# Kernel optimization log

Hardware: AMD Instinct MI355X
Metric: run time of the kernel (lower is better)

## Reference

```python
import jax, jax.numpy as jnp
import numpy as np

HIDDEN = 2048
N_HEADS = 32
N_KV_HEADS = 8
HEAD_DIM = 64
ROPE_THETA = 500000.0
B, S = 1, 2048


def _rope_tables(seq_len):
    inv_freq = 1.0 / ROPE_THETA ** (jnp.arange(0, HEAD_DIM, 2, dtype=jnp.float32) / HEAD_DIM)
    angles = jnp.arange(seq_len, dtype=jnp.float32)[:, None] * inv_freq[None, :]
    return jnp.cos(angles), jnp.sin(angles)


def _apply_rope(x, cos, sin):
    # x: (B, S, H, D); cos/sin: (S, D//2)
    x1 = x[..., 0::2]
    x2 = x[..., 1::2]
    c = cos[None, :, None, :]
    s = sin[None, :, None, :]
    x1r = x1 * c - x2 * s
    x2r = x1 * s + x2 * c
    return jnp.stack([x1r, x2r], axis=-1).reshape(x.shape)


def setup_inputs() -> dict:
    key = jax.random.key(0)
    ks = jax.random.split(key, 5)
    hidden_states = jax.random.normal(ks[0], (B, S, HIDDEN), dtype=jnp.float32)
    # causal mask, broadcastable over (B, H, S, S)
    attention_mask = jnp.tril(jnp.ones((S, S), dtype=bool))[None, :, :]
    sc = 1.0 / np.sqrt(HIDDEN)
    wq = jax.random.normal(ks[1], (HIDDEN, N_HEADS * HEAD_DIM), dtype=jnp.float32) * sc
    wk = jax.random.normal(ks[2], (HIDDEN, N_KV_HEADS * HEAD_DIM), dtype=jnp.float32) * sc
    wv = jax.random.normal(ks[3], (HIDDEN, N_KV_HEADS * HEAD_DIM), dtype=jnp.float32) * sc
    wo = jax.random.normal(ks[4], (N_HEADS * HEAD_DIM, HIDDEN), dtype=jnp.float32) * sc
    return {"hidden_states": hidden_states, "attention_mask": attention_mask,
            "wq": wq, "wk": wk, "wv": wv, "wo": wo}


def reference(hidden_states, attention_mask, wq, wk, wv, wo):
    b, s, _ = hidden_states.shape
    groups = N_HEADS // N_KV_HEADS
    q = (hidden_states @ wq).reshape(b, s, N_HEADS, HEAD_DIM)
    k = (hidden_states @ wk).reshape(b, s, N_KV_HEADS, HEAD_DIM)
    v = (hidden_states @ wv).reshape(b, s, N_KV_HEADS, HEAD_DIM)
    cos, sin = _rope_tables(s)
    q = _apply_rope(q, cos, sin)
    k = _apply_rope(k, cos, sin)
    k = jnp.repeat(k, groups, axis=2)  # (b, s, H, D)
    v = jnp.repeat(v, groups, axis=2)
    q = q.transpose(0, 2, 1, 3)  # (b, H, s, D)
    k = k.transpose(0, 2, 1, 3)
    v = v.transpose(0, 2, 1, 3)
    scores = jnp.einsum('bhqd,bhkd->bhqk', q, k) / jnp.sqrt(jnp.float32(HEAD_DIM))
    scores = jnp.where(attention_mask[:, None, :, :], scores, -jnp.inf)
    probs = jax.nn.softmax(scores, axis=-1)
    out = jnp.einsum('bhqk,bhkd->bhqd', probs, v)
    out = out.transpose(0, 2, 1, 3).reshape(b, s, N_HEADS * HEAD_DIM)
    return out @ wo
```

## Files before the change

### kernel.cpp

```cpp
#include <hip/hip_runtime.h>

typedef __attribute__((ext_vector_type(8))) short short8;
typedef __attribute__((ext_vector_type(4))) float float4v;

__device__ __forceinline__ float bf2f(ushort u) {
    union { uint i; float f; } v; v.i = ((uint)u) << 16; return v.f;
}
__device__ __forceinline__ ushort f2bf(float f) {
    union { uint i; float f; } v; v.f = f;
    return (ushort)((v.i + 0x7FFFu + ((v.i >> 16) & 1u)) >> 16);
}
#if __has_builtin(__builtin_amdgcn_cvt_pk_bf16_f32)
__device__ __forceinline__ uint f2bf_pk(float a, float b) {
    auto r = __builtin_amdgcn_cvt_pk_bf16_f32(a, b);
    return __builtin_bit_cast(uint, r);
}
#else
__device__ __forceinline__ uint f2bf_pk(float a, float b) {
    return (uint)f2bf(a) | ((uint)f2bf(b) << 16);
}
#endif
__device__ __forceinline__ void gld_lds16(const ushort* g, ushort* l) {
    __builtin_amdgcn_global_load_lds((const __attribute__((address_space(1))) unsigned int*)g,
                                     (__attribute__((address_space(3))) unsigned int*)l,
                                     16, 0, 0);
}

__global__ __launch_bounds__(256) void cvt_bf16(const float* __restrict__ in,
                                                ushort* __restrict__ out) {
    const size_t i = ((size_t)blockIdx.x * 256 + threadIdx.x) * 8;
    float4 a = *(const float4*)(in + i);
    float4 b = *(const float4*)(in + i + 4);
    uint4 u;
    u.x = f2bf_pk(a.x, a.y);
    u.y = f2bf_pk(a.z, a.w);
    u.z = f2bf_pk(b.x, b.y);
    u.w = f2bf_pk(b.z, b.w);
    *(uint4*)(out + i) = u;
}

__device__ __forceinline__ void tconv_body(const float* in, ushort* out,
                                           int C, int r0, int c0, int tid) {
    __shared__ float t[64][65];
    const int lrow = tid >> 2;
    const int lc   = (tid & 3) * 16;

    const float* ip = in + (size_t)(r0 + lrow) * C + c0 + lc;
#pragma unroll
    for (int i = 0; i < 4; i++) {
        float4 v = *(const float4*)(ip + 4 * i);
        t[lrow][lc + 4 * i + 0] = v.x; t[lrow][lc + 4 * i + 1] = v.y;
        t[lrow][lc + 4 * i + 2] = v.z; t[lrow][lc + 4 * i + 3] = v.w;
    }
    __syncthreads();
    ushort* op = out + (size_t)(c0 + lrow) * 2048 + r0 + lc;
#pragma unroll
    for (int i = 0; i < 8; i++)
        ((uint*)op)[i] = f2bf_pk(t[lc + 2 * i][lrow], t[lc + 2 * i + 1][lrow]);
}

__global__ __launch_bounds__(256) void tconv(const float* __restrict__ in,
                                             ushort* __restrict__ out) {
    tconv_body(in, out, 2048, blockIdx.y * 64, blockIdx.x * 64, threadIdx.x);
}

__global__ __launch_bounds__(256) void tconv3(const float* __restrict__ wq,
                                              const float* __restrict__ wk,
                                              const float* __restrict__ wv,
                                              ushort* __restrict__ out) {
    const int bx = blockIdx.x;
    const float* in; ushort* op; int C, cx;
    if (bx < 32)      { in = wq; op = out;                          C = 2048; cx = bx; }
    else if (bx < 40) { in = wk; op = out + (size_t)2048 * 2048;    C = 512;  cx = bx - 32; }
    else              { in = wv; op = out + (size_t)2560 * 2048;    C = 512;  cx = bx - 40; }
    tconv_body(in, op, C, blockIdx.y * 64, cx * 64, threadIdx.x);
}

template <bool BF16OUT>
__global__ __launch_bounds__(256) void gemm_n64(const ushort* __restrict__ A,
                                                const ushort* __restrict__ Bt,
                                                void* __restrict__ Cout,
                                                int N, int K) {
    __shared__ ushort As[128 * 32];
    __shared__ ushort Bs[64 * 32];

    const int tid = threadIdx.x, w = tid >> 6, lane = tid & 63;
    const int lr = lane & 15, quad = lane >> 4;
    const int m0 = blockIdx.x * 128, n0 = blockIdx.y * 64;

    const int srow = lane >> 2;
    const int skb  = (lane & 3) ^ ((srow >> 1) & 3);

    float4v acc[2][4];
#pragma unroll
    for (int a = 0; a < 2; a++)
#pragma unroll
        for (int b = 0; b < 4; b++) { acc[a][b][0] = 0.f; acc[a][b][1] = 0.f; acc[a][b][2] = 0.f; acc[a][b][3] = 0.f; }

    const int fsw = (lr >> 1) & 3;

    for (int k0 = 0; k0 < K; k0 += 32) {
        __syncthreads();
#pragma unroll
        for (int i = 0; i < 2; i++) {
            const int rt = 2 * w + i;
            gld_lds16(A + (size_t)(m0 + rt * 16 + srow) * K + k0 + skb * 8, &As[rt * 512]);
        }
        gld_lds16(Bt + (size_t)(n0 + w * 16 + srow) * K + k0 + skb * 8, &Bs[w * 512]);
        __syncthreads();

        short8 af[2], bf[4];
#pragma unroll
        for (int mt = 0; mt < 2; mt++)
            af[mt] = *(const short8*)&As[(w * 32 + mt * 16 + lr) * 32 + (quad ^ fsw) * 8];
#pragma unroll
        for (int nt = 0; nt < 4; nt++)
            bf[nt] = *(const short8*)&Bs[(nt * 16 + lr) * 32 + (quad ^ fsw) * 8];
#pragma unroll
        for (int mt = 0; mt < 2; mt++)
#pragma unroll
            for (int nt = 0; nt < 4; nt++)
                acc[mt][nt] = __builtin_amdgcn_mfma_f32_16x16x32_bf16(af[mt], bf[nt], acc[mt][nt], 0, 0, 0);
    }

    const int rbase = m0 + w * 32 + quad * 4;
    const int cbase = n0 + lr;
#pragma unroll
    for (int mt = 0; mt < 2; mt++)
#pragma unroll
        for (int nt = 0; nt < 4; nt++)
#pragma unroll
            for (int r = 0; r < 4; r++) {
                const size_t idx = (size_t)(rbase + mt * 16 + r) * N + cbase + nt * 16;
                if (BF16OUT) ((ushort*)Cout)[idx] = f2bf(acc[mt][nt][r]);
                else         ((float*)Cout)[idx]  = acc[mt][nt][r];
            }
}

__global__ __launch_bounds__(256) void rope_bf(ushort* __restrict__ Qb,
                                               ushort* __restrict__ Kc) {
    const int idx = blockIdx.x * 256 + threadIdx.x;
    const int QP = 2048 * 1024;
    int s, p; ushort* base; float osc;
    if (idx < QP) { s = idx >> 10; p = idx & 1023; base = Qb; osc = 0.125f; }
    else { int r = idx - QP; s = r >> 8; p = r & 255; base = Kc; osc = 1.0f; }
    const int j = p & 31;
    float inv = __expf(-(float)(2 * j) * (1.0f / 64.0f) * 13.122363377404328f);
    float sn, c;
    sincosf((float)s * inv, &sn, &c);
    uint* p2 = (uint*)(base + (size_t)s * 3072 + 2 * p);
    uint xv = *p2;
    float x1 = bf2f((ushort)(xv & 0xFFFFu)), x2 = bf2f((ushort)(xv >> 16));
    *p2 = f2bf_pk((x1 * c - x2 * sn) * osc, (x1 * sn + x2 * c) * osc);
}

__global__ __launch_bounds__(256) void attn_mfma(const ushort* __restrict__ Q,
                                                 const ushort* __restrict__ Kc,
                                                 const ushort* __restrict__ Vc,
                                                 ushort* __restrict__ O) {
    __shared__ ushort Ks[2][64 * 64];
    __shared__ ushort Vt[2][64 * 72];
    __shared__ ushort Ps[4][16 * 72];

    const int tid = threadIdx.x, w = tid >> 6, lane = tid & 63;
    const int lr = lane & 15, quad = lane >> 4;
    const int h = blockIdx.y, g = h >> 2;

    const int dg = tid & 15;
    const int kl = tid >> 4;
    const int ksub = lane >> 3, dsub = lane & 7;
    ushort* Pw = &Ps[w][0];

    const ushort* Vp0 = Vc + g * 64 + dg * 4 + (size_t)3072 * kl;
    const ushort* Kp0 = Kc + g * 64 + ((dsub ^ ksub) * 8) + (size_t)3072 * ksub;

    short8 onesf;
#pragma unroll
    for (int j = 0; j < 8; j++) onesf[j] = (short)0x3F80;

    for (int ti = 0; ti < 2; ti++) {
        const int bx = ti ? 31 - (int)blockIdx.x : (int)blockIdx.x;

        const ushort* qp = Q + (size_t)(bx * 64 + w * 16 + lr) * 3072 + h * 64 + quad * 8;
        const short8 qf0 = *(const short8*)qp;
        const short8 qf1 = *(const short8*)(qp + 32);

        float4v oacc[4], lacc;
#pragma unroll
        for (int t = 0; t < 4; t++) { oacc[t][0] = 0.f; oacc[t][1] = 0.f; oacc[t][2] = 0.f; oacc[t][3] = 0.f; }
        lacc[0] = 0.f; lacc[1] = 0.f; lacc[2] = 0.f; lacc[3] = 0.f;

        uint2 vv[4];
#pragma unroll
        for (int t = 0; t < 4; t++)
            vv[t] = *(const uint2*)(Vp0 + (size_t)(16 * t) * 3072);
        __syncthreads();
#pragma unroll
        for (int i = 0; i < 2; i++) {
            const int rt = 2 * w + i;
            gld_lds16(Kp0 + (size_t)(rt * 8) * 3072, &Ks[0][rt * 512]);
        }

        for (int kb = 0; kb <= bx; kb++) {
            const int b = kb & 1;
            ushort* bKs = Ks[b];
            ushort* bVt = Vt[b];

#pragma unroll
            for (int i = 0; i < 4; i++) {
                uint e0 = (i < 2) ? vv[0].x : vv[0].y, f0 = (i & 1) ? (e0 >> 16) : (e0 & 0xFFFFu);
                uint e1 = (i < 2) ? vv[1].x : vv[1].y, f1 = (i & 1) ? (e1 >> 16) : (e1 & 0xFFFFu);
                uint e2 = (i < 2) ? vv[2].x : vv[2].y, f2 = (i & 1) ? (e2 >> 16) : (e2 & 0xFFFFu);
                uint e3 = (i < 2) ? vv[3].x : vv[3].y, f3 = (i & 1) ? (e3 >> 16) : (e3 & 0xFFFFu);
                uint2 pk; pk.x = f0 | (f1 << 16); pk.y = f2 | (f3 << 16);
                *(uint2*)&bVt[(dg * 4 + i) * 72 + kl * 4] = pk;
            }

            const int kn = (kb < bx) ? kb + 1 : bx;
#pragma unroll
            for (int t = 0; t < 4; t++)
                vv[t] = *(const uint2*)(Vp0 + (size_t)(kn * 64 + 16 * t) * 3072);

            asm volatile("s_waitcnt vmcnt(4) lgkmcnt(0)\n\ts_barrier" ::: "memory");

#pragma unroll
            for (int i = 0; i < 2; i++) {
                const int rt = 2 * w + i;
                gld_lds16(Kp0 + (size_t)(kn * 64 + rt * 8) * 3072, &Ks[1 - b][rt * 512]);
            }

            float4v sacc[4];
#pragma unroll
            for (int t = 0; t < 4; t++) { sacc[t][0] = 0.f; sacc[t][1] = 0.f; sacc[t][2] = 0.f; sacc[t][3] = 0.f; }
#pragma unroll
            for (int t = 0; t < 4; t++) {
                const int krow = t * 16 + lr;
                const int sw = lr & 7;
                short8 kf0 = *(const short8*)&bKs[krow * 64 + ((quad)     ^ sw) * 8];
                short8 kf1 = *(const short8*)&bKs[krow * 64 + ((quad + 4) ^ sw) * 8];
                sacc[t] = __builtin_amdgcn_mfma_f32_16x16x32_bf16(qf0, kf0, sacc[t], 0, 0, 0);
                sacc[t] = __builtin_amdgcn_mfma_f32_16x16x32_bf16(qf1, kf1, sacc[t], 0, 0, 0);
            }

            const bool mc = (kb == bx);
#pragma unroll
            for (int r = 0; r < 4; r++) {
                const int qr = w * 16 + quad * 4 + r;
                float p[4];
#pragma unroll
                for (int t = 0; t < 4; t++) {
                    float pv = __expf(sacc[t][r]);
                    p[t] = (mc && (t * 16 + lr > qr)) ? 0.f : pv;
                }
                uint2 pk;
                pk.x = f2bf_pk(p[0], p[1]);
                pk.y = f2bf_pk(p[2], p[3]);
                *(uint2*)&Pw[(quad * 4 + r) * 72 + lr * 4] = pk;
            }

#pragma unroll
            for (int ks2 = 0; ks2 < 2; ks2++) {
                short8 pf = *(const short8*)&Pw[lr * 72 + ks2 * 32 + quad * 8];
                lacc = __builtin_amdgcn_mfma_f32_16x16x32_bf16(pf, onesf, lacc, 0, 0, 0);
#pragma unroll
                for (int t = 0; t < 4; t++) {
                    short8 vf = *(const short8*)&bVt[(t * 16 + lr) * 72 + ks2 * 32 + quad * 8];
                    oacc[t] = __builtin_amdgcn_mfma_f32_16x16x32_bf16(pf, vf, oacc[t], 0, 0, 0);
                }
            }
        }

        ushort* op = O + (size_t)(bx * 64 + w * 16 + quad * 4) * 2048 + h * 64 + lr;
#pragma unroll
        for (int t = 0; t < 4; t++)
#pragma unroll
            for (int r = 0; r < 4; r++)
                op[(size_t)r * 2048 + t * 16] = f2bf(oacc[t][r] / lacc[r]);
    }
}

extern "C" void kernel_launch(void* const* d_in, const int* in_sizes, int n_in,
                              void* d_out, int out_size, void* d_ws, size_t ws_size,
                              hipStream_t stream) {
    const float* hidden = (const float*)d_in[0];
    const float* wq = (const float*)d_in[2];
    const float* wk = (const float*)d_in[3];
    const float* wv = (const float*)d_in[4];
    const float* wo = (const float*)d_in[5];

    ushort* ws = (ushort*)d_ws;
    ushort* hid  = ws;
    ushort* wT   = ws + 4194304;
    ushort* QKV  = ws + 10485760;
    ushort* Qb = QKV;
    ushort* Kc = QKV + 2048;
    ushort* Vc = QKV + 2560;
    ushort* Ab = hid;

    cvt_bf16<<<2048, 256, 0, stream>>>(hidden, hid);
    tconv3<<<dim3(48, 32), 256, 0, stream>>>(wq, wk, wv, wT);
    gemm_n64<true><<<dim3(16, 48), 256, 0, stream>>>(hid, wT, QKV, 3072, 2048);
    tconv<<<dim3(32, 32), 256, 0, stream>>>(wo, wT);
    rope_bf<<<10240, 256, 0, stream>>>(Qb, Kc);
    attn_mfma<<<dim3(16, 32), 256, 0, stream>>>(Qb, Kc, Vc, Ab);
    gemm_n64<false><<<dim3(16, 32), 256, 0, stream>>>(Ab, wT, d_out, 2048, 2048);
}
```

Before: 256.6 us.

## Split attention KV blocks across two partitions, merge prep kernels, swizzle LDS

```diff
diff --git a/kernel.cpp b/kernel.cpp
--- a/kernel.cpp
+++ b/kernel.cpp
@@ -2,6 +2,8 @@
 
 typedef __attribute__((ext_vector_type(8))) short short8;
 typedef __attribute__((ext_vector_type(4))) float float4v;
+
+union U4S8 { uint4 u; short8 s; };
 
 __device__ __forceinline__ float bf2f(ushort u) {
     union { uint i; float f; } v; v.i = ((uint)u) << 16; return v.f;
@@ -26,25 +28,11 @@
                                      16, 0, 0);
 }
 
-__global__ __launch_bounds__(256) void cvt_bf16(const float* __restrict__ in,
-                                                ushort* __restrict__ out) {
-    const size_t i = ((size_t)blockIdx.x * 256 + threadIdx.x) * 8;
-    float4 a = *(const float4*)(in + i);
-    float4 b = *(const float4*)(in + i + 4);
-    uint4 u;
-    u.x = f2bf_pk(a.x, a.y);
-    u.y = f2bf_pk(a.z, a.w);
-    u.z = f2bf_pk(b.x, b.y);
-    u.w = f2bf_pk(b.z, b.w);
-    *(uint4*)(out + i) = u;
-}
-
 __device__ __forceinline__ void tconv_body(const float* in, ushort* out,
                                            int C, int r0, int c0, int tid) {
     __shared__ float t[64][65];
     const int lrow = tid >> 2;
     const int lc   = (tid & 3) * 16;
-
     const float* ip = in + (size_t)(r0 + lrow) * C + c0 + lc;
 #pragma unroll
     for (int i = 0; i < 4; i++) {
@@ -59,28 +47,42 @@
         ((uint*)op)[i] = f2bf_pk(t[lc + 2 * i][lrow], t[lc + 2 * i + 1][lrow]);
 }
 
+__global__ __launch_bounds__(256) void prep(const float* __restrict__ hidden,
+                                            const float* __restrict__ wq,
+                                            const float* __restrict__ wk,
+                                            const float* __restrict__ wv,
+                                            ushort* __restrict__ hid,
+                                            ushort* __restrict__ wT) {
+    const int bx = blockIdx.x;
+    if (bx < 2048) {
+        const size_t i = ((size_t)bx * 256 + threadIdx.x) * 8;
+        float4 a = *(const float4*)(hidden + i);
+        float4 b = *(const float4*)(hidden + i + 4);
+        uint4 u;
+        u.x = f2bf_pk(a.x, a.y); u.y = f2bf_pk(a.z, a.w);
+        u.z = f2bf_pk(b.x, b.y); u.w = f2bf_pk(b.z, b.w);
+        *(uint4*)(hid + i) = u;
+    } else {
+        const int i = bx - 2048;
+        const int xx = i % 48, yy = i / 48;
+        const float* in; ushort* op; int C, cx;
+        if (xx < 32)      { in = wq; op = wT;                        C = 2048; cx = xx; }
+        else if (xx < 40) { in = wk; op = wT + (size_t)2048 * 2048;  C = 512;  cx = xx - 32; }
+        else              { in = wv; op = wT + (size_t)2560 * 2048;  C = 512;  cx = xx - 40; }
+        tconv_body(in, op, C, yy * 64, cx * 64, threadIdx.x);
+    }
+}
+
 __global__ __launch_bounds__(256) void tconv(const float* __restrict__ in,
                                              ushort* __restrict__ out) {
     tconv_body(in, out, 2048, blockIdx.y * 64, blockIdx.x * 64, threadIdx.x);
-}
-
-__global__ __launch_bounds__(256) void tconv3(const float* __restrict__ wq,
-                                              const float* __restrict__ wk,
-                                              const float* __restrict__ wv,
-                                              ushort* __restrict__ out) {
-    const int bx = blockIdx.x;
-    const float* in; ushort* op; int C, cx;
-    if (bx < 32)      { in = wq; op = out;                          C = 2048; cx = bx; }
-    else if (bx < 40) { in = wk; op = out + (size_t)2048 * 2048;    C = 512;  cx = bx - 32; }
-    else              { in = wv; op = out + (size_t)2560 * 2048;    C = 512;  cx = bx - 40; }
-    tconv_body(in, op, C, blockIdx.y * 64, cx * 64, threadIdx.x);
 }
 
 template <bool BF16OUT>
 __global__ __launch_bounds__(256) void gemm_n64(const ushort* __restrict__ A,
                                                 const ushort* __restrict__ Bt,
                                                 void* __restrict__ Cout,
-                                                int N, int K) {
+                                                int N, int K, int lda) {
     __shared__ ushort As[128 * 32];
     __shared__ ushort Bs[64 * 32];
 
@@ -104,7 +106,7 @@
 #pragma unroll
         for (int i = 0; i < 2; i++) {
             const int rt = 2 * w + i;
-            gld_lds16(A + (size_t)(m0 + rt * 16 + srow) * K + k0 + skb * 8, &As[rt * 512]);
+            gld_lds16(A + (size_t)(m0 + rt * 16 + srow) * lda + k0 + skb * 8, &As[rt * 512]);
         }
         gld_lds16(Bt + (size_t)(n0 + w * 16 + srow) * K + k0 + skb * 8, &Bs[w * 512]);
         __syncthreads();
@@ -142,7 +144,7 @@
     const int idx = blockIdx.x * 256 + threadIdx.x;
     const int QP = 2048 * 1024;
     int s, p; ushort* base; float osc;
-    if (idx < QP) { s = idx >> 10; p = idx & 1023; base = Qb; osc = 0.125f; }
+    if (idx < QP) { s = idx >> 10; p = idx & 1023; base = Qb; osc = 0.18033688f; }
     else { int r = idx - QP; s = r >> 8; p = r & 255; base = Kc; osc = 1.0f; }
     const int j = p & 31;
     float inv = __expf(-(float)(2 * j) * (1.0f / 64.0f) * 13.122363377404328f);
@@ -157,19 +159,24 @@
 __global__ __launch_bounds__(256) void attn_mfma(const ushort* __restrict__ Q,
                                                  const ushort* __restrict__ Kc,
                                                  const ushort* __restrict__ Vc,
-                                                 ushort* __restrict__ O) {
+                                                 ushort* __restrict__ O0,
+                                                 ushort* __restrict__ O1,
+                                                 float* __restrict__ L0,
+                                                 float* __restrict__ L1) {
     __shared__ ushort Ks[2][64 * 64];
-    __shared__ ushort Vt[2][64 * 72];
-    __shared__ ushort Ps[4][16 * 72];
+    __shared__ ushort Vt[2][64 * 64];
+    __shared__ ushort Ps[4][16 * 64];
 
     const int tid = threadIdx.x, w = tid >> 6, lane = tid & 63;
     const int lr = lane & 15, quad = lane >> 4;
-    const int h = blockIdx.y, g = h >> 2;
+    const int h = blockIdx.y, g = h >> 2, z = blockIdx.z;
 
     const int dg = tid & 15;
     const int kl = tid >> 4;
     const int ksub = lane >> 3, dsub = lane & 7;
-    ushort* Pw = &Ps[w][0];
+    ushort* Pw = Ps[w];
+    ushort* Op = z ? O1 : O0;
+    float*  Lp = z ? L1 : L0;
 
     const ushort* Vp0 = Vc + g * 64 + dg * 4 + (size_t)3072 * kl;
     const ushort* Kp0 = Kc + g * 64 + ((dsub ^ ksub) * 8) + (size_t)3072 * ksub;
@@ -180,6 +187,8 @@
 
     for (int ti = 0; ti < 2; ti++) {
         const int bx = ti ? 31 - (int)blockIdx.x : (int)blockIdx.x;
+        const int nch = (bx >= z) ? ((bx - z) >> 1) + 1 : 0;
+        const int last = z + 2 * (nch - 1);
 
         const ushort* qp = Q + (size_t)(bx * 64 + w * 16 + lr) * 3072 + h * 64 + quad * 8;
         const short8 qf0 = *(const short8*)qp;
@@ -191,32 +200,40 @@
         lacc[0] = 0.f; lacc[1] = 0.f; lacc[2] = 0.f; lacc[3] = 0.f;
 
         uint2 vv[4];
-#pragma unroll
-        for (int t = 0; t < 4; t++)
-            vv[t] = *(const uint2*)(Vp0 + (size_t)(16 * t) * 3072);
+        if (nch) {
+#pragma unroll
+            for (int t = 0; t < 4; t++)
+                vv[t] = *(const uint2*)(Vp0 + (size_t)(z * 64 + 16 * t) * 3072);
+        }
         __syncthreads();
-#pragma unroll
-        for (int i = 0; i < 2; i++) {
-            const int rt = 2 * w + i;
-            gld_lds16(Kp0 + (size_t)(rt * 8) * 3072, &Ks[0][rt * 512]);
-        }
-
-        for (int kb = 0; kb <= bx; kb++) {
-            const int b = kb & 1;
+        if (nch) {
+#pragma unroll
+            for (int i = 0; i < 2; i++) {
+                const int rt = 2 * w + i;
+                gld_lds16(Kp0 + (size_t)(z * 64 + rt * 8) * 3072, &Ks[0][rt * 512]);
+            }
+        }
+
+        for (int c = 0; c < nch; c++) {
+            const int kb = z + 2 * c;
+            const int b = c & 1;
             ushort* bKs = Ks[b];
             ushort* bVt = Vt[b];
 
 #pragma unroll
             for (int i = 0; i < 4; i++) {
-                uint e0 = (i < 2) ? vv[0].x : vv[0].y, f0 = (i & 1) ? (e0 >> 16) : (e0 & 0xFFFFu);
-                uint e1 = (i < 2) ? vv[1].x : vv[1].y, f1 = (i & 1) ? (e1 >> 16) : (e1 & 0xFFFFu);
-                uint e2 = (i < 2) ? vv[2].x : vv[2].y, f2 = (i & 1) ? (e2 >> 16) : (e2 & 0xFFFFu);
-                uint e3 = (i < 2) ? vv[3].x : vv[3].y, f3 = (i & 1) ? (e3 >> 16) : (e3 & 0xFFFFu);
-                uint2 pk; pk.x = f0 | (f1 << 16); pk.y = f2 | (f3 << 16);
-                *(uint2*)&bVt[(dg * 4 + i) * 72 + kl * 4] = pk;
-            }
-
-            const int kn = (kb < bx) ? kb + 1 : bx;
+                const uint sel = (i & 1) ? 0x07060302u : 0x05040100u;
+                uint s0 = (i < 2) ? vv[0].x : vv[0].y;
+                uint s1 = (i < 2) ? vv[1].x : vv[1].y;
+                uint s2 = (i < 2) ? vv[2].x : vv[2].y;
+                uint s3 = (i < 2) ? vv[3].x : vv[3].y;
+                uint2 pk;
+                pk.x = __builtin_amdgcn_perm(s1, s0, sel);
+                pk.y = __builtin_amdgcn_perm(s3, s2, sel);
+                *(uint2*)&bVt[(dg * 4 + i) * 64 + (kl ^ ((dg & 3) * 4 + i)) * 4] = pk;
+            }
+
+            const int kn = (c + 1 < nch) ? kb + 2 : last;
 #pragma unroll
             for (int t = 0; t < 4; t++)
                 vv[t] = *(const uint2*)(Vp0 + (size_t)(kn * 64 + 16 * t) * 3072);
@@ -242,41 +259,88 @@
                 sacc[t] = __builtin_amdgcn_mfma_f32_16x16x32_bf16(qf1, kf1, sacc[t], 0, 0, 0);
             }
 
-            const bool mc = (kb == bx);
-#pragma unroll
-            for (int r = 0; r < 4; r++) {
-                const int qr = w * 16 + quad * 4 + r;
-                float p[4];
+            if (kb == bx) {
+#pragma unroll
+                for (int r = 0; r < 4; r++) {
+                    const int qr = w * 16 + quad * 4 + r;
+                    float p0 = exp2f(sacc[0][r]), p1 = exp2f(sacc[1][r]);
+                    float p2 = exp2f(sacc[2][r]), p3 = exp2f(sacc[3][r]);
+                    if (lr > qr)      p0 = 0.f;
+                    if (16 + lr > qr) p1 = 0.f;
+                    if (32 + lr > qr) p2 = 0.f;
+                    if (48 + lr > qr) p3 = 0.f;
+                    const int prow = quad * 4 + r;
+                    uint2 pk; pk.x = f2bf_pk(p0, p1); pk.y = f2bf_pk(p2, p3);
+                    *(uint2*)&Pw[prow * 64 + (lr ^ prow) * 4] = pk;
+                }
+            } else {
+#pragma unroll
+                for (int r = 0; r < 4; r++) {
+                    const int prow = quad * 4 + r;
+                    uint2 pk;
+                    pk.x = f2bf_pk(exp2f(sacc[0][r]), exp2f(sacc[1][r]));
+                    pk.y = f2bf_pk(exp2f(sacc[2][r]), exp2f(sacc[3][r]));
+                    *(uint2*)&Pw[prow * 64 + (lr ^ prow) * 4] = pk;
+                }
+            }
+
+#pragma unroll
+            for (int ks2 = 0; ks2 < 2; ks2++) {
+                const int ub = ks2 * 8 + quad * 2;
+                U4S8 pu;
+                uint2 plo = *(const uint2*)&Pw[lr * 64 + ((ub)     ^ lr) * 4];
+                uint2 phi = *(const uint2*)&Pw[lr * 64 + ((ub + 1) ^ lr) * 4];
+                pu.u.x = plo.x; pu.u.y = plo.y; pu.u.z = phi.x; pu.u.w = phi.y;
+                lacc = __builtin_amdgcn_mfma_f32_16x16x32_bf16(pu.s, onesf, lacc, 0, 0, 0);
 #pragma unroll
                 for (int t = 0; t < 4; t++) {
-                    float pv = __expf(sacc[t][r]);
-                    p[t] = (mc && (t * 16 + lr > qr)) ? 0.f : pv;
+                    const int d = t * 16 + lr;
+                    U4S8 vu;
+                    uint2 vlo = *(const uint2*)&bVt[d * 64 + ((ub)     ^ lr) * 4];
+                    uint2 vhi = *(const uint2*)&bVt[d * 64 + ((ub + 1) ^ lr) * 4];
+                    vu.u.x = vlo.x; vu.u.y = vlo.y; vu.u.z = vhi.x; vu.u.w = vhi.y;
+                    oacc[t] = __builtin_amdgcn_mfma_f32_16x16x32_bf16(pu.s, vu.s, oacc[t], 0, 0, 0);
                 }
-                uint2 pk;
-                pk.x = f2bf_pk(p[0], p[1]);
-                pk.y = f2bf_pk(p[2], p[3]);
-                *(uint2*)&Pw[(quad * 4 + r) * 72 + lr * 4] = pk;
-            }
-
-#pragma unroll
-            for (int ks2 = 0; ks2 < 2; ks2++) {
-                short8 pf = *(const short8*)&Pw[lr * 72 + ks2 * 32 + quad * 8];
-                lacc = __builtin_amdgcn_mfma_f32_16x16x32_bf16(pf, onesf, lacc, 0, 0, 0);
-#pragma unroll
-                for (int t = 0; t < 4; t++) {
-                    short8 vf = *(const short8*)&bVt[(t * 16 + lr) * 72 + ks2 * 32 + quad * 8];
-                    oacc[t] = __builtin_amdgcn_mfma_f32_16x16x32_bf16(pf, vf, oacc[t], 0, 0, 0);
-                }
-            }
-        }
-
-        ushort* op = O + (size_t)(bx * 64 + w * 16 + quad * 4) * 2048 + h * 64 + lr;
+            }
+        }
+
+        ushort* op = Op + (size_t)(bx * 64 + w * 16 + quad * 4) * 2048 + h * 64 + lr;
 #pragma unroll
         for (int t = 0; t < 4; t++)
 #pragma unroll
             for (int r = 0; r < 4; r++)
-                op[(size_t)r * 2048 + t * 16] = f2bf(oacc[t][r] / lacc[r]);
-    }
+                op[(size_t)r * 2048 + t * 16] = f2bf(oacc[t][r]);
+        if (lr == 0) {
+#pragma unroll
+            for (int r = 0; r < 4; r++)
+                Lp[h * 2048 + bx * 64 + w * 16 + quad * 4 + r] = lacc[r];
+        }
+    }
+}
+
+__global__ __launch_bounds__(256) void combine(const ushort* __restrict__ O0,
+                                               const ushort* __restrict__ O1,
+                                               const float* __restrict__ L0,
+                                               const float* __restrict__ L1,
+                                               ushort* __restrict__ Ab) {
+    const int idx = blockIdx.x * 256 + threadIdx.x;
+    const int r = idx >> 8;
+    const int c8 = (idx & 255) * 8;
+    const int h = c8 >> 6;
+    const float rl = 1.0f / (L0[h * 2048 + r] + L1[h * 2048 + r]);
+    uint4 a = *(const uint4*)(O0 + (size_t)r * 2048 + c8);
+    uint4 b = *(const uint4*)(O1 + (size_t)r * 2048 + c8);
+    uint ua[4] = {a.x, a.y, a.z, a.w}, ub[4] = {b.x, b.y, b.z, b.w};
+    uint4 res;
+    uint rr[4];
+#pragma unroll
+    for (int k = 0; k < 4; k++) {
+        float x0 = bf2f((ushort)(ua[k] & 0xFFFFu)) + bf2f((ushort)(ub[k] & 0xFFFFu));
+        float x1 = bf2f((ushort)(ua[k] >> 16))     + bf2f((ushort)(ub[k] >> 16));
+        rr[k] = f2bf_pk(x0 * rl, x1 * rl);
+    }
+    res.x = rr[0]; res.y = rr[1]; res.z = rr[2]; res.w = rr[3];
+    *(uint4*)(Ab + (size_t)r * 3072 + c8) = res;
 }
 
 extern "C" void kernel_launch(void* const* d_in, const int* in_sizes, int n_in,
@@ -295,13 +359,15 @@
     ushort* Qb = QKV;
     ushort* Kc = QKV + 2048;
     ushort* Vc = QKV + 2560;
-    ushort* Ab = hid;
-
-    cvt_bf16<<<2048, 256, 0, stream>>>(hidden, hid);
-    tconv3<<<dim3(48, 32), 256, 0, stream>>>(wq, wk, wv, wT);
-    gemm_n64<true><<<dim3(16, 48), 256, 0, stream>>>(hid, wT, QKV, 3072, 2048);
+    ushort* O1 = (ushort*)d_out;
+    float*  L0 = (float*)((ushort*)d_out + 4194304);
+    float*  L1 = L0 + 65536;
+
+    prep<<<3584, 256, 0, stream>>>(hidden, wq, wk, wv, hid, wT);
+    gemm_n64<true><<<dim3(16, 48), 256, 0, stream>>>(hid, wT, QKV, 3072, 2048, 2048);
     tconv<<<dim3(32, 32), 256, 0, stream>>>(wo, wT);
     rope_bf<<<10240, 256, 0, stream>>>(Qb, Kc);
-    attn_mfma<<<dim3(16, 32), 256, 0, stream>>>(Qb, Kc, Vc, Ab);
-    gemm_n64<false><<<dim3(16, 32), 256, 0, stream>>>(Ab, wT, d_out, 2048, 2048);
-}
+    attn_mfma<<<dim3(16, 32, 2), 256, 0, stream>>>(Qb, Kc, Vc, hid , O1, L0, L1);
+    combine<<<2048, 256, 0, stream>>>(hid, O1, L0, L1, Qb );
+    gemm_n64<false><<<dim3(16, 32), 256, 0, stream>>>(Qb, wT, d_out, 2048, 2048, 3072);
+}
```

Measured after the change: 251.9 us. About the same (-1.8%).
